# Performance work log

Measured on AMD Instinct MI355X. Metric: run time of the kernel, lower is better.

The kernel has to match this reference:

```python
import jax, jax.numpy as jnp
import numpy as np

BATCH = 4096
MAX_ATOMS = 1024


def setup_inputs() -> dict:
    key = jax.random.key(0)
    k1, k2, k3 = jax.random.split(key, 3)
    inp = jax.random.normal(k1, (BATCH, 3 * MAX_ATOMS), dtype=jnp.float32)
    tgt = jax.random.normal(k2, (BATCH, 3 * MAX_ATOMS), dtype=jnp.float32)
    num_atoms = jax.random.randint(k3, (BATCH,), 8, MAX_ATOMS + 1, dtype=jnp.int32)
    return {"input": inp, "target": tgt, "num_atoms": num_atoms}


def _kabsch_rmsd(inp, tgt, num_atoms):
    B = inp.shape[0]
    N = inp.shape[1] // 3
    x = inp.reshape(B, N, 3)
    y = tgt.reshape(B, N, 3)
    # mask out padded atoms (atom index >= num_atoms)
    mask = (jnp.arange(N)[None, :] < num_atoms[:, None])[..., None]  # [B,N,1]
    n = num_atoms.astype(x.dtype)[:, None, None]                      # [B,1,1]
    xm = jnp.where(mask, x, 0.0)
    ym = jnp.where(mask, y, 0.0)
    # center on masked centroid; keep padded rows exactly zero
    xc = jnp.where(mask, xm - xm.sum(axis=1, keepdims=True) / n, 0.0)
    yc = jnp.where(mask, ym - ym.sum(axis=1, keepdims=True) / n, 0.0)
    # 3x3 covariance per sample
    R = jnp.einsum("bni,bnj->bij", xc, yc)
    U, S, Vt = jnp.linalg.svd(R)
    # proper-rotation (reflection) correction
    d = jnp.sign(jnp.linalg.det(U) * jnp.linalg.det(Vt))
    s = S[:, 0] + S[:, 1] + d * S[:, 2]
    e = (jnp.sum(xc * xc, axis=(1, 2)) + jnp.sum(yc * yc, axis=(1, 2)) - 2.0 * s)
    msd = e / num_atoms.astype(e.dtype)
    return jnp.sqrt(jnp.maximum(msd, 1e-12))


def reference(input, target, num_atoms):
    return _kabsch_rmsd(input, target, num_atoms)
```

## Files before the change

### kernel.cpp

```cpp
#include <hip/hip_runtime.h>
#include <math.h>

constexpr int NATOMS = 1024;

__device__ __forceinline__ float wred(float v) {
#pragma unroll
    for (int o = 32; o > 0; o >>= 1) v += __shfl_xor(v, o, 64);
    return v;
}

__global__ __launch_bounds__(256) void rmsd_kernel(
    const float* __restrict__ inp, const float* __restrict__ tgt,
    const int* __restrict__ natoms, float* __restrict__ out)
{
    const int b = blockIdx.x;
    const int t = threadIdx.x;
    const int n = natoms[b];

    const float4* __restrict__ x4 = (const float4*)(inp + (size_t)b * (3 * NATOMS)) + t * 3;
    const float4* __restrict__ y4 = (const float4*)(tgt + (size_t)b * (3 * NATOMS)) + t * 3;

    float4 xa = x4[0], xb = x4[1], xc = x4[2];
    float4 ya = y4[0], yb = y4[1], yc = y4[2];

    float acc[17];
#pragma unroll
    for (int i = 0; i < 17; ++i) acc[i] = 0.f;

    const float X[4][3] = {{xa.x,xa.y,xa.z},{xa.w,xb.x,xb.y},{xb.z,xb.w,xc.x},{xc.y,xc.z,xc.w}};
    const float Y[4][3] = {{ya.x,ya.y,ya.z},{ya.w,yb.x,yb.y},{yb.z,yb.w,yc.x},{yc.y,yc.z,yc.w}};
    const int base = t * 4;
#pragma unroll
    for (int j = 0; j < 4; ++j) {
        const float m = (base + j < n) ? 1.f : 0.f;
        const float x0 = X[j][0]*m, x1 = X[j][1]*m, x2 = X[j][2]*m;
        const float y0 = Y[j][0]*m, y1 = Y[j][1]*m, y2 = Y[j][2]*m;
        acc[0] += x0; acc[1] += x1; acc[2] += x2;
        acc[3] += y0; acc[4] += y1; acc[5] += y2;
        acc[6]  += x0*y0; acc[7]  += x0*y1; acc[8]  += x0*y2;
        acc[9]  += x1*y0; acc[10] += x1*y1; acc[11] += x1*y2;
        acc[12] += x2*y0; acc[13] += x2*y1; acc[14] += x2*y2;
        acc[15] += x0*x0 + x1*x1 + x2*x2;
        acc[16] += y0*y0 + y1*y1 + y2*y2;
    }

#pragma unroll
    for (int i = 0; i < 17; ++i) acc[i] = wred(acc[i]);

    __shared__ float red[4][17];
    const int wave = t >> 6, lane = t & 63;
    if (lane == 0) {
#pragma unroll
        for (int i = 0; i < 17; ++i) red[wave][i] = acc[i];
    }
    __syncthreads();

    if (t == 0) {
        double s[17];
#pragma unroll
        for (int i = 0; i < 17; ++i)
            s[i] = (double)red[0][i] + (double)red[1][i] + (double)red[2][i] + (double)red[3][i];
        const double nd = (double)n;

        double R[3][3];
        for (int i = 0; i < 3; ++i)
            for (int j = 0; j < 3; ++j)
                R[i][j] = s[6 + i*3 + j] - s[i] * s[3 + j] / nd;
        const double ex = s[15] - (s[0]*s[0] + s[1]*s[1] + s[2]*s[2]) / nd;
        const double ey = s[16] - (s[3]*s[3] + s[4]*s[4] + s[5]*s[5]) / nd;

        const double detR =
              R[0][0]*(R[1][1]*R[2][2] - R[1][2]*R[2][1])
            - R[0][1]*(R[1][0]*R[2][2] - R[1][2]*R[2][0])
            + R[0][2]*(R[1][0]*R[2][1] - R[1][1]*R[2][0]);

        double K00=0, K01=0, K02=0, K11=0, K12=0, K22=0;
        for (int k = 0; k < 3; ++k) {
            K00 += R[k][0]*R[k][0]; K01 += R[k][0]*R[k][1]; K02 += R[k][0]*R[k][2];
            K11 += R[k][1]*R[k][1]; K12 += R[k][1]*R[k][2]; K22 += R[k][2]*R[k][2];
        }

        const double qm = (K00 + K11 + K22) / 3.0;
        const double p1 = K01*K01 + K02*K02 + K12*K12;
        const double p2 = (K00-qm)*(K00-qm) + (K11-qm)*(K11-qm) + (K22-qm)*(K22-qm) + 2.0*p1;
        double e1, e2, e3;
        if (p2 <= 1e-30) {
            e1 = e2 = e3 = qm;
        } else {
            const double p = sqrt(p2 / 6.0);
            const double inv = 1.0 / p;
            const double B00 = (K00-qm)*inv, B11 = (K11-qm)*inv, B22 = (K22-qm)*inv;
            const double B01 = K01*inv, B02 = K02*inv, B12 = K12*inv;
            const double detB =
                  B00*(B11*B22 - B12*B12)
                - B01*(B01*B22 - B12*B02)
                + B02*(B01*B12 - B11*B02);
            double r = detB * 0.5;
            r = fmin(1.0, fmax(-1.0, r));
            const double phi = acos(r) / 3.0;
            e1 = qm + 2.0*p*cos(phi);
            e3 = qm + 2.0*p*cos(phi + 2.0943951023931953);
            e2 = 3.0*qm - e1 - e3;
        }
        const double S1 = sqrt(fmax(e1, 0.0));
        const double S2 = sqrt(fmax(e2, 0.0));
        const double S3 = sqrt(fmax(e3, 0.0));
        const double dsg = (detR < 0.0) ? -1.0 : 1.0;
        const double sv = S1 + S2 + dsg * S3;

        const double e = ex + ey - 2.0 * sv;
        out[b] = (float)sqrt(fmax(e / nd, 1e-12));
    }
}

extern "C" void kernel_launch(void* const* d_in, const int* in_sizes, int n_in,
                              void* d_out, int out_size, void* d_ws, size_t ws_size,
                              hipStream_t stream) {
    const float* inp = (const float*)d_in[0];
    const float* tgt = (const float*)d_in[1];
    const int*   na  = (const int*)d_in[2];
    float* out = (float*)d_out;
    const int batch = in_sizes[2];
    rmsd_kernel<<<batch, 256, 0, stream>>>(inp, tgt, na, out);
}
```

Before: 118.9 us.

## Map one wave per sample and skip loads for padded atoms

Each 64-lane wave now processes one batch sample, so a block handles four samples and no longer needs shared-memory reduction or a block barrier. Loads of atom groups beyond num_atoms are skipped entirely, cutting memory traffic for padded rows. The two sum-of-squares accumulators are merged into one. Each lane now reads a contiguous 16-atom chunk, which makes per-instruction access less coalesced than the previous layout.

```diff
diff --git a/kernel.cpp b/kernel.cpp
--- a/kernel.cpp
+++ b/kernel.cpp
@@ -1,73 +1,67 @@
 #include <hip/hip_runtime.h>
 #include <math.h>
 
-constexpr int NATOMS = 1024;
-
-__device__ __forceinline__ float wred(float v) {
-#pragma unroll
-    for (int o = 32; o > 0; o >>= 1) v += __shfl_xor(v, o, 64);
-    return v;
-}
-
 __global__ __launch_bounds__(256) void rmsd_kernel(
     const float* __restrict__ inp, const float* __restrict__ tgt,
-    const int* __restrict__ natoms, float* __restrict__ out)
+    const int* __restrict__ natoms, float* __restrict__ out, int batch)
 {
-    const int b = blockIdx.x;
-    const int t = threadIdx.x;
+    const int wave = threadIdx.x >> 6;
+    const int lane = threadIdx.x & 63;
+    const int b = blockIdx.x * 4 + wave;
+    if (b >= batch) return;
     const int n = natoms[b];
 
-    const float4* __restrict__ x4 = (const float4*)(inp + (size_t)b * (3 * NATOMS)) + t * 3;
-    const float4* __restrict__ y4 = (const float4*)(tgt + (size_t)b * (3 * NATOMS)) + t * 3;
+    const float4* __restrict__ x4 = (const float4*)(inp + (size_t)b * 3072);
+    const float4* __restrict__ y4 = (const float4*)(tgt + (size_t)b * 3072);
 
-    float4 xa = x4[0], xb = x4[1], xc = x4[2];
-    float4 ya = y4[0], yb = y4[1], yc = y4[2];
+    float acc[16];
+#pragma unroll
+    for (int i = 0; i < 16; ++i) acc[i] = 0.f;
 
-    float acc[17];
 #pragma unroll
-    for (int i = 0; i < 17; ++i) acc[i] = 0.f;
-
-    const float X[4][3] = {{xa.x,xa.y,xa.z},{xa.w,xb.x,xb.y},{xb.z,xb.w,xc.x},{xc.y,xc.z,xc.w}};
-    const float Y[4][3] = {{ya.x,ya.y,ya.z},{ya.w,yb.x,yb.y},{yb.z,yb.w,yc.x},{yc.y,yc.z,yc.w}};
-    const int base = t * 4;
+    for (int g = 0; g < 4; ++g) {
+        const int a0 = lane * 16 + g * 4;
+        if (a0 < n) {
+            const int f = lane * 12 + g * 3;
+            const float4 xa = x4[f], xb = x4[f + 1], xc = x4[f + 2];
+            const float4 ya = y4[f], yb = y4[f + 1], yc = y4[f + 2];
+            const float X[4][3] = {{xa.x,xa.y,xa.z},{xa.w,xb.x,xb.y},
+                                   {xb.z,xb.w,xc.x},{xc.y,xc.z,xc.w}};
+            const float Y[4][3] = {{ya.x,ya.y,ya.z},{ya.w,yb.x,yb.y},
+                                   {yb.z,yb.w,yc.x},{yc.y,yc.z,yc.w}};
 #pragma unroll
-    for (int j = 0; j < 4; ++j) {
-        const float m = (base + j < n) ? 1.f : 0.f;
-        const float x0 = X[j][0]*m, x1 = X[j][1]*m, x2 = X[j][2]*m;
-        const float y0 = Y[j][0]*m, y1 = Y[j][1]*m, y2 = Y[j][2]*m;
-        acc[0] += x0; acc[1] += x1; acc[2] += x2;
-        acc[3] += y0; acc[4] += y1; acc[5] += y2;
-        acc[6]  += x0*y0; acc[7]  += x0*y1; acc[8]  += x0*y2;
-        acc[9]  += x1*y0; acc[10] += x1*y1; acc[11] += x1*y2;
-        acc[12] += x2*y0; acc[13] += x2*y1; acc[14] += x2*y2;
-        acc[15] += x0*x0 + x1*x1 + x2*x2;
-        acc[16] += y0*y0 + y1*y1 + y2*y2;
+            for (int j = 0; j < 4; ++j) {
+                const float m = (a0 + j < n) ? 1.f : 0.f;
+                const float x0 = X[j][0]*m, x1 = X[j][1]*m, x2 = X[j][2]*m;
+                const float y0 = Y[j][0]*m, y1 = Y[j][1]*m, y2 = Y[j][2]*m;
+                acc[0] += x0; acc[1] += x1; acc[2] += x2;
+                acc[3] += y0; acc[4] += y1; acc[5] += y2;
+                acc[6]  += x0*y0; acc[7]  += x0*y1; acc[8]  += x0*y2;
+                acc[9]  += x1*y0; acc[10] += x1*y1; acc[11] += x1*y2;
+                acc[12] += x2*y0; acc[13] += x2*y1; acc[14] += x2*y2;
+                acc[15] += x0*x0 + x1*x1 + x2*x2 + y0*y0 + y1*y1 + y2*y2;
+            }
+        }
     }
 
 #pragma unroll
-    for (int i = 0; i < 17; ++i) acc[i] = wred(acc[i]);
+    for (int o = 32; o > 0; o >>= 1) {
+#pragma unroll
+        for (int i = 0; i < 16; ++i) acc[i] += __shfl_xor(acc[i], o, 64);
+    }
 
-    __shared__ float red[4][17];
-    const int wave = t >> 6, lane = t & 63;
     if (lane == 0) {
+        double s[16];
 #pragma unroll
-        for (int i = 0; i < 17; ++i) red[wave][i] = acc[i];
-    }
-    __syncthreads();
-
-    if (t == 0) {
-        double s[17];
-#pragma unroll
-        for (int i = 0; i < 17; ++i)
-            s[i] = (double)red[0][i] + (double)red[1][i] + (double)red[2][i] + (double)red[3][i];
+        for (int i = 0; i < 16; ++i) s[i] = (double)acc[i];
         const double nd = (double)n;
 
         double R[3][3];
         for (int i = 0; i < 3; ++i)
             for (int j = 0; j < 3; ++j)
                 R[i][j] = s[6 + i*3 + j] - s[i] * s[3 + j] / nd;
-        const double ex = s[15] - (s[0]*s[0] + s[1]*s[1] + s[2]*s[2]) / nd;
-        const double ey = s[16] - (s[3]*s[3] + s[4]*s[4] + s[5]*s[5]) / nd;
+        const double exy = s[15] - (s[0]*s[0] + s[1]*s[1] + s[2]*s[2]
+                                  + s[3]*s[3] + s[4]*s[4] + s[5]*s[5]) / nd;
 
         const double detR =
               R[0][0]*(R[1][1]*R[2][2] - R[1][2]*R[2][1])
@@ -82,7 +76,8 @@
 
         const double qm = (K00 + K11 + K22) / 3.0;
         const double p1 = K01*K01 + K02*K02 + K12*K12;
-        const double p2 = (K00-qm)*(K00-qm) + (K11-qm)*(K11-qm) + (K22-qm)*(K22-qm) + 2.0*p1;
+        const double p2 = (K00-qm)*(K00-qm) + (K11-qm)*(K11-qm)
+                        + (K22-qm)*(K22-qm) + 2.0*p1;
         double e1, e2, e3;
         if (p2 <= 1e-30) {
             e1 = e2 = e3 = qm;
@@ -108,7 +103,7 @@
         const double dsg = (detR < 0.0) ? -1.0 : 1.0;
         const double sv = S1 + S2 + dsg * S3;
 
-        const double e = ex + ey - 2.0 * sv;
+        const double e = exy - 2.0 * sv;
         out[b] = (float)sqrt(fmax(e / nd, 1e-12));
     }
 }
@@ -121,5 +116,5 @@
     const int*   na  = (const int*)d_in[2];
     float* out = (float*)d_out;
     const int batch = in_sizes[2];
-    rmsd_kernel<<<batch, 256, 0, stream>>>(inp, tgt, na, out);
+    rmsd_kernel<<<(batch + 3) / 4, 256, 0, stream>>>(inp, tgt, na, out, batch);
 }
```

Result: slower. 128.0 us (+7.7%).
